# Kernel tuning notes

Measured on AMD Instinct MI355X. Metric: run time of the kernel, lower is better.

## Reference

```python
import jax, jax.numpy as jnp
import numpy as np

N_NODES = 50000
N_EDGES = 800000
DIM = 256
DEPTH = 4
N_REL = 4
EPS = 1e-5


def setup_inputs() -> dict:
    key = jax.random.key(0)
    ks = jax.random.split(key, 8)
    scale = 1.0 / np.sqrt(DIM)
    return {
        "node_embedding": jax.random.normal(ks[0], (N_NODES, DIM), jnp.float32),
        "weights": jax.random.normal(ks[1], (DEPTH, N_REL, DIM, DIM), jnp.float32) * scale,
        "roots": jax.random.normal(ks[2], (DEPTH, DIM, DIM), jnp.float32) * scale,
        "biases": jax.random.normal(ks[3], (DEPTH, DIM), jnp.float32) * 0.01,
        "ln_gamma": jnp.ones((DEPTH, DIM), jnp.float32),
        "ln_beta": jnp.zeros((DEPTH, DIM), jnp.float32),
        "edge_index": jax.random.randint(ks[4], (2, N_EDGES), 0, N_NODES, jnp.int32),
        "edge_type": jax.random.randint(ks[5], (N_EDGES,), 0, N_REL, jnp.int32),
    }


def _rgcn_layer(X, W, root, bias, gamma, beta, src, dst, etype, inv_deg):
    # RGCNConv with aggr='mean': per-relation transform, then per-relation mean
    # over incoming edges at the target node, summed across relations.
    h = jnp.einsum('ni,rio->rno', X, W)            # [R, N, D]
    msg = h[etype, src] * inv_deg[:, None]         # [E, D] gather + per-relation 1/deg
    agg = jax.ops.segment_sum(msg, dst, num_segments=X.shape[0])  # [N, D]
    out = agg + X @ root + bias
    # LayerNorm
    mu = jnp.mean(out, axis=-1, keepdims=True)
    var = jnp.mean(jnp.square(out - mu), axis=-1, keepdims=True)
    out = (out - mu) * jax.lax.rsqrt(var + EPS) * gamma + beta
    out = jax.nn.elu(out)
    return out + X  # residual connection (dropout p=0 -> identity)


def reference(node_embedding, weights, roots, biases, ln_gamma, ln_beta, edge_index, edge_type):
    src, dst = edge_index[0], edge_index[1]
    # per-(node, relation) in-degree for the relation-wise mean aggregation
    cnt = jnp.zeros((node_embedding.shape[0], N_REL), node_embedding.dtype)
    cnt = cnt.at[dst, edge_type].add(1.0)
    inv_deg = 1.0 / jnp.maximum(cnt[dst, edge_type], 1.0)  # [E]
    X = node_embedding
    for l in range(DEPTH):
        X = _rgcn_layer(X, weights[l], roots[l], biases[l], ln_gamma[l], ln_beta[l],
                        src, dst, edge_type, inv_deg)
    return X
```

## Files before the change

### kernel.cpp

```cpp
#include <hip/hip_runtime.h>
#include <hip/hip_bf16.h>
#include <stdint.h>

#define NN 50000
#define NE 800000
#define DD 256
#define NL 4
#define NRL 4
#define KT 1280
#define KA 1024

typedef float f32x4 __attribute__((ext_vector_type(4)));
typedef __bf16 bf16x8 __attribute__((ext_vector_type(8)));
typedef __bf16 bf16x4 __attribute__((ext_vector_type(4)));
typedef unsigned short u16x4 __attribute__((ext_vector_type(4)));

static __device__ __forceinline__ unsigned short f2bf(float f) {
  __bf16 h = (__bf16)f;
  return __builtin_bit_cast(unsigned short, h);
}

static __device__ __forceinline__ u16x4 pk4(f32x4 v) {
  u16x4 o;
  o.x = f2bf(v.x); o.y = f2bf(v.y); o.z = f2bf(v.z); o.w = f2bf(v.w);
  return o;
}

static __device__ __forceinline__ void async16(const void* g, void* l) {
  __builtin_amdgcn_global_load_lds(
      (const __attribute__((address_space(1))) unsigned int*)g,
      (__attribute__((address_space(3))) unsigned int*)l, 16, 0, 0);
}

static __device__ __forceinline__ void async16nt(const void* g, void* l) {
  __builtin_amdgcn_global_load_lds(
      (const __attribute__((address_space(1))) unsigned int*)g,
      (__attribute__((address_space(3))) unsigned int*)l, 16, 0, 2);
}


__global__ __launch_bounds__(256) void k_hist(const int* __restrict__ ei,
                                              const int* __restrict__ et,
                                              int* __restrict__ cntNR) {
  int e = blockIdx.x * 256 + threadIdx.x;
  if (e >= NE) return;
  int dst = ei[NE + e];
  int r = et[e];
  atomicAdd(&cntNR[dst * 4 + r], 1);
}

__global__ __launch_bounds__(256) void k_scan1(const int* __restrict__ cntNR,
                                               int* __restrict__ offs,
                                               int* __restrict__ bsum) {
  __shared__ int sd[256];
  const int t = threadIdx.x;
  const int n = blockIdx.x * 256 + t;
  int deg = 0;
  if (n < NN) {
    const int* c = cntNR + n * 4;
    deg = c[0] + c[1] + c[2] + c[3];
  }
  sd[t] = deg;
  __syncthreads();
  int val = deg;
  for (int d = 1; d < 256; d <<= 1) {
    int other = (t >= d) ? sd[t - d] : 0;
    __syncthreads();
    val += other;
    sd[t] = val;
    __syncthreads();
  }
  if (n < NN) offs[n] = val - deg;
  if (t == 255) bsum[blockIdx.x] = val;
}

__global__ __launch_bounds__(256) void k_scan2(const int* __restrict__ bsum,
                                               int* __restrict__ boff, int nb) {
  __shared__ int sd[256];
  const int t = threadIdx.x;
  int v = (t < nb) ? bsum[t] : 0;
  sd[t] = v;
  __syncthreads();
  int val = v;
  for (int d = 1; d < 256; d <<= 1) {
    int other = (t >= d) ? sd[t - d] : 0;
    __syncthreads();
    val += other;
    sd[t] = val;
    __syncthreads();
  }
  boff[t] = val - v;
}

__global__ __launch_bounds__(256) void k_scan3(int* __restrict__ offs,
                                               const int* __restrict__ boff,
                                               int* __restrict__ cursor) {
  int n = blockIdx.x * 256 + threadIdx.x;
  if (n < NN) {
    int o = offs[n] + boff[blockIdx.x];
    offs[n] = o;
    cursor[n] = o;
  }
  if (n == 0) offs[NN] = NE;
}

__global__ __launch_bounds__(256) void k_scatter(const int* __restrict__ ei,
                                                 const int* __restrict__ et,
                                                 int* __restrict__ cursor,
                                                 uint32_t* __restrict__ packed) {
  int e = blockIdx.x * 256 + threadIdx.x;
  if (e >= NE) return;
  int src = ei[e];
  int dst = ei[NE + e];
  int r = et[e];
  int pos = atomicAdd(&cursor[dst], 1);
  packed[pos] = (uint32_t)src | ((uint32_t)r << 16);
}

__global__ __launch_bounds__(256) void k_wconv(const float* __restrict__ weights,
                                               const float* __restrict__ roots,
                                               __hip_bfloat16* __restrict__ WbigT) {
  int idx = blockIdx.x * 256 + threadIdx.x;
  if (idx >= NL * DD * KT) return;
  int l = idx / (DD * KT);
  int rem = idx - l * (DD * KT);
  int o = rem / KT;
  int k = rem - o * KT;
  float v;
  if (k < NRL * DD) {
    int r = k >> 8, i = k & 255;
    v = weights[(((size_t)(l * NRL + r) * DD) + i) * DD + o];
  } else {
    int i = k - NRL * DD;
    v = roots[((size_t)l * DD + i) * DD + o];
  }
  WbigT[idx] = __float2bfloat16(v);
}

__global__ __launch_bounds__(256) void k_cast(const float* __restrict__ X,
                                              __hip_bfloat16* __restrict__ Xbf) {
  int i = blockIdx.x * 256 + threadIdx.x;
  if (i >= NN * 64) return;
  const f32x4* Xv = (const f32x4*)X;
  ((u16x4*)Xbf)[i] = pk4(Xv[i]);
}


__global__ __launch_bounds__(256) void k_agg(const __hip_bfloat16* __restrict__ Xbf,
                                             const uint32_t* __restrict__ packed,
                                             const int* __restrict__ offs,
                                             const int* __restrict__ cntNR,
                                             __hip_bfloat16* __restrict__ Abig) {
  const int wid = (blockIdx.x * 256 + threadIdx.x) >> 6;
  const int lane = threadIdx.x & 63;
  if (wid >= NN) return;
  const int beg = offs[wid];
  const int end = offs[wid + 1];
  const bf16x4* __restrict__ Xv = (const bf16x4*)Xbf;

  f32x4 a0 = {0.f, 0.f, 0.f, 0.f}, a1 = a0, a2 = a0, a3 = a0;

  for (int e = beg; e < end; e += 8) {
    uint32_t pv[8];
    bf16x4 vv[8];
#pragma unroll
    for (int i = 0; i < 8; ++i) {
      int ee = e + i;
      ee = (ee < end) ? ee : (end - 1);
      pv[i] = packed[ee];
    }
#pragma unroll
    for (int i = 0; i < 8; ++i) {
      vv[i] = Xv[(int)(pv[i] & 0xFFFFu) * 64 + lane];
    }
    const int nv = end - e;
#pragma unroll
    for (int i = 0; i < 8; ++i) {
      if (i < nv) {
        int r = (int)(pv[i] >> 16);
        f32x4 v = {(float)vv[i][0], (float)vv[i][1], (float)vv[i][2], (float)vv[i][3]};
        if (r == 0) a0 += v;
        else if (r == 1) a1 += v;
        else if (r == 2) a2 += v;
        else a3 += v;
      }
    }
  }

  const int* c = cntNR + wid * 4;
  int c0 = c[0], c1 = c[1], c2 = c[2], c3 = c[3];
  float s0 = 1.0f / (float)(c0 > 1 ? c0 : 1);
  float s1 = 1.0f / (float)(c1 > 1 ? c1 : 1);
  float s2 = 1.0f / (float)(c2 > 1 ? c2 : 1);
  float s3 = 1.0f / (float)(c3 > 1 ? c3 : 1);

  u16x4* Arow = (u16x4*)(Abig + (size_t)wid * KA);
  __builtin_nontemporal_store(pk4(a0 * s0), Arow + 0 * 64 + lane);
  __builtin_nontemporal_store(pk4(a1 * s1), Arow + 1 * 64 + lane);
  __builtin_nontemporal_store(pk4(a2 * s2), Arow + 2 * 64 + lane);
  __builtin_nontemporal_store(pk4(a3 * s3), Arow + 3 * 64 + lane);
}


__global__ __launch_bounds__(256) void k_gemm(const __hip_bfloat16* __restrict__ A,
                                              const __hip_bfloat16* __restrict__ Xbf_in,
                                              const __hip_bfloat16* __restrict__ Bt,
                                              const float* __restrict__ bias,
                                              const float* __restrict__ gamma,
                                              const float* __restrict__ beta,
                                              const float* __restrict__ Xin,
                                              float* __restrict__ Xout,
                                              __hip_bfloat16* __restrict__ Xbf_out) {
  __shared__ __align__(16) char sA[128 * 64];
  __shared__ __align__(16) char sB[256 * 64];
  __shared__ float sRed[128][4];

  const int tid = threadIdx.x;
  const int w = tid >> 6;
  const int lane = tid & 63;
  const int wm = w >> 1, wn = w & 1;
  const int quad = lane >> 4, l15 = lane & 15;
  const int mBase = blockIdx.x * 128;

  const int srow = lane >> 2;
  const int kc = (lane & 3) ^ ((lane >> 3) & 3);

  int am0 = mBase + w * 32 + srow;
  int am1 = am0 + 16;
  if (am0 >= NN) am0 = NN - 1;
  if (am1 >= NN) am1 = NN - 1;
  const char* agp0 = (const char*)A + (size_t)am0 * (KA * 2) + kc * 16;
  const char* agp1 = (const char*)A + (size_t)am1 * (KA * 2) + kc * 16;
  const char* agx0 = (const char*)Xbf_in + (size_t)am0 * (DD * 2) + kc * 16;
  const char* agx1 = (const char*)Xbf_in + (size_t)am1 * (DD * 2) + kc * 16;
  const char* bgp0 = (const char*)Bt + (size_t)(w * 64 + 0 + srow) * (KT * 2) + kc * 16;
  const char* bgp1 = (const char*)Bt + (size_t)(w * 64 + 16 + srow) * (KT * 2) + kc * 16;
  const char* bgp2 = (const char*)Bt + (size_t)(w * 64 + 32 + srow) * (KT * 2) + kc * 16;
  const char* bgp3 = (const char*)Bt + (size_t)(w * 64 + 48 + srow) * (KT * 2) + kc * 16;
  char* alp0 = sA + w * 2048;
  char* alp1 = sA + w * 2048 + 1024;
  char* blp0 = sB + w * 4096 + 0;
  char* blp1 = sB + w * 4096 + 1024;
  char* blp2 = sB + w * 4096 + 2048;
  char* blp3 = sB + w * 4096 + 3072;

  f32x4 acc[4][8];
#pragma unroll
  for (int i = 0; i < 4; ++i)
#pragma unroll
    for (int j = 0; j < 8; ++j) acc[i][j] = (f32x4){0.f, 0.f, 0.f, 0.f};

  const int aslot = (quad ^ ((l15 >> 1) & 3)) * 16;
  const char* aAddr = sA + (wm * 64 + l15) * 64 + aslot;
  const char* bAddr = sB + (wn * 128 + l15) * 64 + aslot;

  for (int k0 = 0; k0 < KT * 2; k0 += 64) {
    __syncthreads();
    if (k0 < KA * 2) {
      async16nt(agp0 + k0, alp0);
      async16nt(agp1 + k0, alp1);
    } else {
      const int kx = k0 - KA * 2;
      async16(agx0 + kx, alp0);
      async16(agx1 + kx, alp1);
    }
    async16(bgp0 + k0, blp0);
    async16(bgp1 + k0, blp1);
    async16(bgp2 + k0, blp2);
    async16(bgp3 + k0, blp3);
    __syncthreads();
    bf16x8 a0 = *(const bf16x8*)(aAddr + 0 * 1024);
    bf16x8 a1 = *(const bf16x8*)(aAddr + 1 * 1024);
    bf16x8 a2 = *(const bf16x8*)(aAddr + 2 * 1024);
    bf16x8 a3 = *(const bf16x8*)(aAddr + 3 * 1024);
#pragma unroll
    for (int nt = 0; nt < 8; ++nt) {
      bf16x8 b = *(const bf16x8*)(bAddr + nt * 1024);
      acc[0][nt] = __builtin_amdgcn_mfma_f32_16x16x32_bf16(a0, b, acc[0][nt], 0, 0, 0);
      acc[1][nt] = __builtin_amdgcn_mfma_f32_16x16x32_bf16(a1, b, acc[1][nt], 0, 0, 0);
      acc[2][nt] = __builtin_amdgcn_mfma_f32_16x16x32_bf16(a2, b, acc[2][nt], 0, 0, 0);
      acc[3][nt] = __builtin_amdgcn_mfma_f32_16x16x32_bf16(a3, b, acc[3][nt], 0, 0, 0);
    }
  }

  float bv[8], gv[8], bev[8];
#pragma unroll
  for (int nt = 0; nt < 8; ++nt) {
    int n = wn * 128 + nt * 16 + l15;
    bv[nt] = bias[n];
    gv[nt] = gamma[n];
    bev[nt] = beta[n];
  }

#pragma unroll
  for (int mt = 0; mt < 4; ++mt) {
#pragma unroll
    for (int reg = 0; reg < 4; ++reg) {
      float s = 0.f, q = 0.f;
#pragma unroll
      for (int nt = 0; nt < 8; ++nt) {
        float v = acc[mt][nt][reg] + bv[nt];
        acc[mt][nt][reg] = v;
        s += v;
        q += v * v;
      }
#pragma unroll
      for (int d = 1; d < 16; d <<= 1) {
        s += __shfl_xor(s, d, 64);
        q += __shfl_xor(q, d, 64);
      }
      if (l15 == 0) {
        int row = wm * 64 + mt * 16 + quad * 4 + reg;
        sRed[row][wn * 2] = s;
        sRed[row][wn * 2 + 1] = q;
      }
    }
  }
  __syncthreads();

#pragma unroll
  for (int mt = 0; mt < 4; ++mt) {
#pragma unroll
    for (int reg = 0; reg < 4; ++reg) {
      int row = wm * 64 + mt * 16 + quad * 4 + reg;
      float ts = sRed[row][0] + sRed[row][2];
      float tq = sRed[row][1] + sRed[row][3];
      float mean = ts * (1.0f / 256.0f);
      float var = tq * (1.0f / 256.0f) - mean * mean;
      float rstd = rsqrtf(var + 1e-5f);
      int m = mBase + row;
      if (m < NN) {
#pragma unroll
        for (int nt = 0; nt < 8; ++nt) {
          int n = wn * 128 + nt * 16 + l15;
          float v = (acc[mt][nt][reg] - mean) * rstd * gv[nt] + bev[nt];
          v = v > 0.0f ? v : (__expf(v) - 1.0f);
          float res = v + Xin[(size_t)m * 256 + n];
          Xout[(size_t)m * 256 + n] = res;
          Xbf_out[(size_t)m * 256 + n] = __float2bfloat16(res);
        }
      }
    }
  }
}


extern "C" void kernel_launch(void* const* d_in, const int* in_sizes, int n_in,
                              void* d_out, int out_size, void* d_ws, size_t ws_size,
                              hipStream_t stream) {
  const float* X0 = (const float*)d_in[0];
  const float* weights = (const float*)d_in[1];
  const float* roots = (const float*)d_in[2];
  const float* biases = (const float*)d_in[3];
  const float* ln_g = (const float*)d_in[4];
  const float* ln_b = (const float*)d_in[5];
  const int* eidx = (const int*)d_in[6];
  const int* etyp = (const int*)d_in[7];
  float* out = (float*)d_out;

  char* ws = (char*)d_ws;
  size_t off = 0;
  auto alloc = [&](size_t bytes) -> char* {
    char* p = ws + off;
    off = (off + bytes + 255) & ~(size_t)255;
    return p;
  };
  __hip_bfloat16* Abig = (__hip_bfloat16*)alloc((size_t)NN * KA * 2);
  __hip_bfloat16* WbigT = (__hip_bfloat16*)alloc((size_t)NL * DD * KT * 2);
  float* Xb0 = (float*)alloc((size_t)NN * DD * 4);
  float* Xb1 = (float*)alloc((size_t)NN * DD * 4);
  __hip_bfloat16* Xbf0 = (__hip_bfloat16*)alloc((size_t)NN * DD * 2);
  __hip_bfloat16* Xbf1 = (__hip_bfloat16*)alloc((size_t)NN * DD * 2);
  int* cntNR = (int*)alloc((size_t)NN * 4 * 4);
  int* offs = (int*)alloc((size_t)(NN + 1) * 4);
  int* cursor = (int*)alloc((size_t)NN * 4);
  uint32_t* packed = (uint32_t*)alloc((size_t)NE * 4);
  int* bsum = (int*)alloc(256 * 4);
  int* boff = (int*)alloc(256 * 4);
  (void)ws_size; (void)in_sizes; (void)n_in; (void)out_size;

  (void)hipMemsetAsync(cntNR, 0, (size_t)NN * 16, stream);
  k_hist<<<(NE + 255) / 256, 256, 0, stream>>>(eidx, etyp, cntNR);
  const int NB = (NN + 255) / 256;
  k_scan1<<<NB, 256, 0, stream>>>(cntNR, offs, bsum);
  k_scan2<<<1, 256, 0, stream>>>(bsum, boff, NB);
  k_scan3<<<NB, 256, 0, stream>>>(offs, boff, cursor);
  k_scatter<<<(NE + 255) / 256, 256, 0, stream>>>(eidx, etyp, cursor, packed);
  k_wconv<<<(NL * DD * KT + 255) / 256, 256, 0, stream>>>(weights, roots, WbigT);
  k_cast<<<(NN * 64 + 255) / 256, 256, 0, stream>>>(X0, Xbf0);

  const float* Xin = X0;
  for (int l = 0; l < NL; ++l) {
    float* Xout = (l == NL - 1) ? out : ((l & 1) ? Xb1 : Xb0);
    const __hip_bfloat16* Xbin = (l & 1) ? Xbf1 : Xbf0;
    __hip_bfloat16* Xbout = (l & 1) ? Xbf0 : Xbf1;
    k_agg<<<(NN * 64 + 255) / 256, 256, 0, stream>>>(Xbin, packed, offs, cntNR, Abig);
    k_gemm<<<(NN + 127) / 128, 256, 0, stream>>>(Abig, Xbin,
                                                 WbigT + (size_t)l * DD * KT,
                                                 biases + (size_t)l * DD,
                                                 ln_g + (size_t)l * DD,
                                                 ln_b + (size_t)l * DD, Xin, Xout, Xbout);
    Xin = Xout;
  }
}
```

Baseline: 970.5 us.

## Double-buffer GEMM LDS tiles and adjust nontemporal hints on A and X

The fused GEMM now keeps two LDS buffers for the A and B tiles and issues the async global-to-LDS loads for the next K step before computing on the current one. This lets load latency overlap with the MFMA work, and each iteration needs one barrier instead of two. The gather kernel's A stores and the GEMM's A loads become normal cached accesses instead of nontemporal ones, likely so A stays in cache between the two kernels. The residual read of X and the fp32 output store are switched to nontemporal. Doubling the A/B LDS footprint may lower occupancy, and relying on the hardware's vmcnt ordering with only one barrier per step adds some correctness risk.

Result: slower. 1.020 ms (+5.1%).

```diff
diff --git a/kernel.cpp b/kernel.cpp
--- a/kernel.cpp
+++ b/kernel.cpp
@@ -30,12 +30,6 @@
   __builtin_amdgcn_global_load_lds(
       (const __attribute__((address_space(1))) unsigned int*)g,
       (__attribute__((address_space(3))) unsigned int*)l, 16, 0, 0);
-}
-
-static __device__ __forceinline__ void async16nt(const void* g, void* l) {
-  __builtin_amdgcn_global_load_lds(
-      (const __attribute__((address_space(1))) unsigned int*)g,
-      (__attribute__((address_space(3))) unsigned int*)l, 16, 0, 2);
 }
 
 
@@ -195,12 +189,14 @@
   float s3 = 1.0f / (float)(c3 > 1 ? c3 : 1);
 
   u16x4* Arow = (u16x4*)(Abig + (size_t)wid * KA);
-  __builtin_nontemporal_store(pk4(a0 * s0), Arow + 0 * 64 + lane);
-  __builtin_nontemporal_store(pk4(a1 * s1), Arow + 1 * 64 + lane);
-  __builtin_nontemporal_store(pk4(a2 * s2), Arow + 2 * 64 + lane);
-  __builtin_nontemporal_store(pk4(a3 * s3), Arow + 3 * 64 + lane);
-}
-
+  Arow[0 * 64 + lane] = pk4(a0 * s0);
+  Arow[1 * 64 + lane] = pk4(a1 * s1);
+  Arow[2 * 64 + lane] = pk4(a2 * s2);
+  Arow[3 * 64 + lane] = pk4(a3 * s3);
+}
+
+
+#define NITER 40
 
 __global__ __launch_bounds__(256) void k_gemm(const __hip_bfloat16* __restrict__ A,
                                               const __hip_bfloat16* __restrict__ Xbf_in,
@@ -211,8 +207,8 @@
                                               const float* __restrict__ Xin,
                                               float* __restrict__ Xout,
                                               __hip_bfloat16* __restrict__ Xbf_out) {
-  __shared__ __align__(16) char sA[128 * 64];
-  __shared__ __align__(16) char sB[256 * 64];
+  __shared__ __align__(16) char sA[2][128 * 64];
+  __shared__ __align__(16) char sB[2][256 * 64];
   __shared__ float sRed[128][4];
 
   const int tid = threadIdx.x;
@@ -237,45 +233,51 @@
   const char* bgp1 = (const char*)Bt + (size_t)(w * 64 + 16 + srow) * (KT * 2) + kc * 16;
   const char* bgp2 = (const char*)Bt + (size_t)(w * 64 + 32 + srow) * (KT * 2) + kc * 16;
   const char* bgp3 = (const char*)Bt + (size_t)(w * 64 + 48 + srow) * (KT * 2) + kc * 16;
-  char* alp0 = sA + w * 2048;
-  char* alp1 = sA + w * 2048 + 1024;
-  char* blp0 = sB + w * 4096 + 0;
-  char* blp1 = sB + w * 4096 + 1024;
-  char* blp2 = sB + w * 4096 + 2048;
-  char* blp3 = sB + w * 4096 + 3072;
-
-  f32x4 acc[4][8];
-#pragma unroll
-  for (int i = 0; i < 4; ++i)
-#pragma unroll
-    for (int j = 0; j < 8; ++j) acc[i][j] = (f32x4){0.f, 0.f, 0.f, 0.f};
-
-  const int aslot = (quad ^ ((l15 >> 1) & 3)) * 16;
-  const char* aAddr = sA + (wm * 64 + l15) * 64 + aslot;
-  const char* bAddr = sB + (wn * 128 + l15) * 64 + aslot;
-
-  for (int k0 = 0; k0 < KT * 2; k0 += 64) {
-    __syncthreads();
+
+  auto stage = [&](int it, int p) {
+    const int k0 = it * 64;
+    char* alp0 = sA[p] + w * 2048;
+    char* alp1 = sA[p] + w * 2048 + 1024;
     if (k0 < KA * 2) {
-      async16nt(agp0 + k0, alp0);
-      async16nt(agp1 + k0, alp1);
+      async16(agp0 + k0, alp0);
+      async16(agp1 + k0, alp1);
     } else {
       const int kx = k0 - KA * 2;
       async16(agx0 + kx, alp0);
       async16(agx1 + kx, alp1);
     }
-    async16(bgp0 + k0, blp0);
-    async16(bgp1 + k0, blp1);
-    async16(bgp2 + k0, blp2);
-    async16(bgp3 + k0, blp3);
+    char* blp = sB[p] + w * 4096;
+    async16(bgp0 + k0, blp + 0);
+    async16(bgp1 + k0, blp + 1024);
+    async16(bgp2 + k0, blp + 2048);
+    async16(bgp3 + k0, blp + 3072);
+  };
+
+  f32x4 acc[4][8];
+#pragma unroll
+  for (int i = 0; i < 4; ++i)
+#pragma unroll
+    for (int j = 0; j < 8; ++j) acc[i][j] = (f32x4){0.f, 0.f, 0.f, 0.f};
+
+  const int aslot = (quad ^ ((l15 >> 1) & 3)) * 16;
+  const int aOff = (wm * 64 + l15) * 64 + aslot;
+  const int bOff = (wn * 128 + l15) * 64 + aslot;
+
+  stage(0, 0);
+
+  for (int it = 0; it < NITER; ++it) {
+    const int p = it & 1;
     __syncthreads();
-    bf16x8 a0 = *(const bf16x8*)(aAddr + 0 * 1024);
-    bf16x8 a1 = *(const bf16x8*)(aAddr + 1 * 1024);
-    bf16x8 a2 = *(const bf16x8*)(aAddr + 2 * 1024);
-    bf16x8 a3 = *(const bf16x8*)(aAddr + 3 * 1024);
+    if (it + 1 < NITER) stage(it + 1, p ^ 1);
+    const char* aB = sA[p] + aOff;
+    const char* bB = sB[p] + bOff;
+    bf16x8 a0 = *(const bf16x8*)(aB + 0 * 1024);
+    bf16x8 a1 = *(const bf16x8*)(aB + 1 * 1024);
+    bf16x8 a2 = *(const bf16x8*)(aB + 2 * 1024);
+    bf16x8 a3 = *(const bf16x8*)(aB + 3 * 1024);
 #pragma unroll
     for (int nt = 0; nt < 8; ++nt) {
-      bf16x8 b = *(const bf16x8*)(bAddr + nt * 1024);
+      bf16x8 b = *(const bf16x8*)(bB + nt * 1024);
       acc[0][nt] = __builtin_amdgcn_mfma_f32_16x16x32_bf16(a0, b, acc[0][nt], 0, 0, 0);
       acc[1][nt] = __builtin_amdgcn_mfma_f32_16x16x32_bf16(a1, b, acc[1][nt], 0, 0, 0);
       acc[2][nt] = __builtin_amdgcn_mfma_f32_16x16x32_bf16(a2, b, acc[2][nt], 0, 0, 0);
@@ -335,8 +337,8 @@
           int n = wn * 128 + nt * 16 + l15;
           float v = (acc[mt][nt][reg] - mean) * rstd * gv[nt] + bev[nt];
           v = v > 0.0f ? v : (__expf(v) - 1.0f);
-          float res = v + Xin[(size_t)m * 256 + n];
-          Xout[(size_t)m * 256 + n] = res;
+          float res = v + __builtin_nontemporal_load(Xin + (size_t)m * 256 + n);
+          __builtin_nontemporal_store(res, Xout + (size_t)m * 256 + n);
           Xbf_out[(size_t)m * 256 + n] = __float2bfloat16(res);
         }
       }
```
